# Optimization experiments

Hardware: AMD Instinct MI355X
Metric: run time of the kernel (lower is better)

The kernel has to match this reference:

```python
import jax, jax.numpy as jnp
import numpy as np

B, E, D, P, H = 8192, 100, 300, 100, 20  # batch, experts, embed, projection, hidden

def setup_inputs() -> dict:
    key = jax.random.key(0)
    ks = jax.random.split(key, 10)
    return {
        "x": jax.random.normal(ks[0], (B, D), dtype=jnp.float32),
        "y": jax.random.normal(ks[1], (B, D), dtype=jnp.float32),
        "tag": jax.random.uniform(ks[2], (B, 1), dtype=jnp.float32),
        "weights_1": jax.random.normal(ks[3], (E, D, P), dtype=jnp.float32) * (2.0 / (D + P)) ** 0.5,
        "bias_1": jax.random.normal(ks[4], (E, P), dtype=jnp.float32) * 0.1,
        "hidden_weights": jax.random.normal(ks[5], (E, 2 * P + 2, H), dtype=jnp.float32) * 0.07,
        "hidden_bias": jax.random.normal(ks[6], (E, H), dtype=jnp.float32),
        "outlayer_weights": jax.random.normal(ks[7], (E, H, 1), dtype=jnp.float32) * 0.3,
        "outlayer_bias": jax.random.uniform(ks[8], (E, 1), dtype=jnp.float32),
        "weights_all": jax.random.normal(ks[9], (D, E), dtype=jnp.float32) * (2.0 / (D + E)) ** 0.5,
    }

def reference(x, y, tag, weights_1, bias_1, hidden_weights, hidden_bias,
              outlayer_weights, outlayer_bias, weights_all):
    eps = 1e-8
    # gating: softmax((x+y) @ W_all) over experts  -> [B, E, 1]
    w = jax.nn.softmax((x + y) @ weights_all, axis=1)[:, :, None]
    # per-expert projections: [B, E, P]
    xp = jnp.einsum('bd,edp->bep', x, weights_1) + bias_1
    yp = jnp.einsum('bd,edp->bep', y, weights_1) + bias_1
    # cosine similarity along projection dim (torch semantics: clamp each norm)
    nx = jnp.maximum(jnp.sqrt(jnp.sum(xp * xp, axis=2)), eps)
    ny = jnp.maximum(jnp.sqrt(jnp.sum(yp * yp, axis=2)), eps)
    cos = jnp.sum(xp * yp, axis=2) / (nx * ny)  # [B, E]
    tag_rep = jnp.broadcast_to(tag[:, None, :], (x.shape[0], weights_1.shape[0], tag.shape[1]))
    feat = jnp.concatenate([cos[:, :, None], xp + yp, jnp.abs(xp - yp), tag_rep], axis=2)  # [B,E,2P+2]
    h = jax.nn.relu(jnp.einsum('bef,efh->beh', feat, hidden_weights) + hidden_bias)  # [B,E,H]
    d = jnp.einsum('beh,eho->beo', h, outlayer_weights) + outlayer_bias  # [B,E,1]
    probs = jnp.squeeze(jnp.sum(w * d, axis=1), axis=-1)  # [B]
    return probs
```

## Files before the change

kernel.cpp:

```cpp
#include <hip/hip_runtime.h>
#include <math.h>

#define B_ 8192
#define E_ 100
#define D_ 300
#define P_ 100
#define H_ 20
#define F_ 202
#define NT 10
#define NWG 12800

typedef __attribute__((ext_vector_type(8))) short bf16x8;
typedef __attribute__((ext_vector_type(8))) _Float16 f16x8;
typedef __attribute__((ext_vector_type(4))) float f32x4;
typedef __attribute__((ext_vector_type(8))) unsigned short us8;

#define WG_OFF 0
#define AB_OFF 3276800
#define W1_OFF (AB_OFF + 20971520)
#define WH2_OFF (W1_OFF + 14336000)
#define PD_OFF (WH2_OFF + 1856000)
#define WS_ALL (PD_OFF + 3276800)

__device__ __forceinline__ unsigned short f2bf(float f) {
    unsigned int u = __float_as_uint(f);
    u = (u + 0x7FFF + ((u >> 16) & 1)) >> 16;
    return (unsigned short)u;
}
__device__ __forceinline__ float bf2f(unsigned short h) {
    return __uint_as_float(((unsigned int)h) << 16);
}

#define GLOAD16(g, l) \
    __builtin_amdgcn_global_load_lds((const __attribute__((address_space(1))) unsigned int*)(g), \
                                     (__attribute__((address_space(3))) unsigned int*)(l), 16, 0, 0)

__global__ __launch_bounds__(256) void prep_xy(const float* __restrict__ x,
                                               const float* __restrict__ y,
                                               unsigned short* __restrict__ ab2)
{
    const int bi = blockIdx.x;
    const int rb = bi / NT, t = bi - rb * NT;
    for (int s = threadIdx.x; s < 512; s += 256) {
        const int kg = s >> 7, row = s & 127;
        const float* src = ((row < 64) ? x : y) + (size_t)(rb * 64 + (row & 63)) * D_;
        const int k0 = t * 32 + kg * 8;
        us8 hi, lo;
        #pragma unroll
        for (int j = 0; j < 8; ++j) {
            const int k = k0 + j;
            const float v = (k < D_) ? src[k] : 0.f;
            const unsigned short h = f2bf(v);
            hi[j] = h;
            lo[j] = f2bf(v - bf2f(h));
        }
        unsigned short* tb = ab2 + (size_t)bi * 8192;
        *(us8*)(tb + (size_t)s * 8)         = hi;
        *(us8*)(tb + (size_t)(512 + s) * 8) = lo;
    }
}

__global__ __launch_bounds__(256) void prep_w1(const float* __restrict__ w1,
                                               unsigned short* __restrict__ w1b2)
{
    const int bi = blockIdx.x;
    const int e = bi / NT, t = bi - e * NT;
    for (int s = threadIdx.x; s < 448; s += 256) {
        const int kg = s / 112, p = s - kg * 112;
        const int k0 = t * 32 + kg * 8;
        us8 hi, lo;
        #pragma unroll
        for (int j = 0; j < 8; ++j) {
            const int k = k0 + j;
            const float v = (p < P_ && k < D_) ? w1[((size_t)e * D_ + k) * P_ + p] : 0.f;
            const unsigned short h = f2bf(v);
            hi[j] = h;
            lo[j] = f2bf(v - bf2f(h));
        }
        unsigned short* tb = w1b2 + (size_t)bi * 7168;
        *(us8*)(tb + (size_t)s * 8)         = hi;
        *(us8*)(tb + (size_t)(448 + s) * 8) = lo;
    }
}

__global__ __launch_bounds__(256) void prep_wh(const float* __restrict__ wh,
                                               _Float16* __restrict__ wh2)
{
    const int e = blockIdx.x;
    for (int k = threadIdx.x; k < 20 * 232; k += 256) {
        const int h = k / 232, f = k - h * 232;
        const float v = (f < F_) ? wh[((size_t)e * F_ + f) * H_ + h] : 0.f;
        const _Float16 vh = (_Float16)v;
        wh2[(size_t)e * 9280 + k]        = vh;
        wh2[(size_t)e * 9280 + 4640 + k] = (_Float16)(v - (float)vh);
    }
}

__global__ __launch_bounds__(128) void gate_kernel(
    const float* __restrict__ x, const float* __restrict__ y,
    const float* __restrict__ wall, float* __restrict__ wgate)
{
    __shared__ float s[D_];
    __shared__ float zv[128];
    __shared__ float red[128];
    const int b = blockIdx.x;
    const int tid = threadIdx.x;

    for (int d = tid; d < D_; d += 128)
        s[d] = x[(size_t)b * D_ + d] + y[(size_t)b * D_ + d];
    __syncthreads();

    float acc = 0.f;
    if (tid < E_)
        for (int d = 0; d < D_; ++d) acc += s[d] * wall[(size_t)d * E_ + tid];
    zv[tid] = (tid < E_) ? acc : -INFINITY;
    red[tid] = zv[tid];
    __syncthreads();
    for (int st = 64; st > 0; st >>= 1) {
        if (tid < st) red[tid] = fmaxf(red[tid], red[tid + st]);
        __syncthreads();
    }
    const float m = red[0];
    __syncthreads();
    const float ev = (tid < E_) ? expf(zv[tid] - m) : 0.f;
    red[tid] = ev;
    __syncthreads();
    for (int st = 64; st > 0; st >>= 1) {
        if (tid < st) red[tid] += red[tid + st];
        __syncthreads();
    }
    if (tid < E_) wgate[(size_t)b * E_ + tid] = ev / red[0];
}

template<int MODE>
__global__ __launch_bounds__(256, (MODE == 1) ? 4 : 3) void moe_mfma_kernel(
    const float* __restrict__ tag,
    const unsigned short* __restrict__ ab2,
    const unsigned short* __restrict__ w1b2,
    const _Float16* __restrict__ wh2g,
    const float* __restrict__ b1,
    const float* __restrict__ wh,
    const float* __restrict__ hb,
    const float* __restrict__ wo,
    const float* __restrict__ ob,
    const float* __restrict__ wgate,
    float* __restrict__ pd,
    float* __restrict__ out)
{
    __shared__ __align__(16) char smem[(MODE == 1) ? 29696 : 48256];
    unsigned short (*Bw_lds)[7168] = (unsigned short (*)[7168])smem;
    _Float16 (*featl)[232] = (_Float16 (*)[232])smem;
    _Float16 (*swh2)[20][232] = (_Float16 (*)[20][232])(smem + 29696);

    const int tid  = threadIdx.x;
    const int lane = tid & 63, w = tid >> 6;

    const int bid = blockIdx.x;
    const int rb = ((bid & 7) << 4) | ((bid >> 3) & 15);
    const int e  = bid >> 7;
    const int b0 = rb * 64;
    const int li = lane & 15, kgq = lane >> 4;

    if constexpr (MODE == 0) {
        for (int k = tid; k < 20 * 232; k += 256) {
            const int h = k / 232, f = k - h * 232;
            const float v = (f < F_) ? wh[((size_t)e * F_ + f) * H_ + h] : 0.f;
            const _Float16 vh = (_Float16)v;
            (*swh2)[h][f] = vh;
            swh2[1][h][f] = (_Float16)(v - (float)vh);
        }
    }

    f32x4 accx[7], accy[7];
    #pragma unroll
    for (int ni = 0; ni < 7; ++ni) {
        accx[ni] = (f32x4){0.f, 0.f, 0.f, 0.f};
        accy[ni] = (f32x4){0.f, 0.f, 0.f, 0.f};
    }

    const int a_base = (kgq * 128 + w * 16 + li) * 8;
    const int b_base = (kgq * 112 + li) * 8;

    bf16x8 areg[2][4];
    auto loadA = [&](int kt, int pb) {
        const unsigned short* tb = ab2 + (size_t)(rb * NT + kt) * 8192 + a_base;
        areg[pb][0] = *(const bf16x8*)(tb);
        areg[pb][1] = *(const bf16x8*)(tb + 4096);
        areg[pb][2] = *(const bf16x8*)(tb + 512);
        areg[pb][3] = *(const bf16x8*)(tb + 4608);
    };
    auto stageB = [&](int tt, int bb) {
        const unsigned short* bbase = w1b2 + (size_t)(e * NT + tt) * 7168 + lane * 8;
        #pragma unroll
        for (int k = 0; k < 4; ++k) {
            const int i = w + 4 * k;
            if (i < 14) GLOAD16(bbase + i * 512, &Bw_lds[bb][i * 512]);
        }
    };

    stageB(0, 0);
    loadA(0, 0);
    __syncthreads();
    #pragma unroll
    for (int kt = 0; kt < NT; ++kt) {
        const int cb = kt & 1, nb = cb ^ 1;
        if (kt < NT - 1) {
            stageB(kt + 1, nb);
            loadA(kt + 1, nb);
        }
        const bf16x8 axh = areg[cb][0];
        const bf16x8 axl = areg[cb][1];
        const bf16x8 ayh = areg[cb][2];
        const bf16x8 ayl = areg[cb][3];
        #pragma unroll
        for (int ni = 0; ni < 7; ++ni) {
            const bf16x8 bh = *(const bf16x8*)(&Bw_lds[cb][b_base + ni * 128]);
            const bf16x8 bl = *(const bf16x8*)(&Bw_lds[cb][b_base + ni * 128 + 3584]);
            accx[ni] = __builtin_amdgcn_mfma_f32_16x16x32_bf16(axh, bh, accx[ni], 0, 0, 0);
            accx[ni] = __builtin_amdgcn_mfma_f32_16x16x32_bf16(axl, bh, accx[ni], 0, 0, 0);
            accx[ni] = __builtin_amdgcn_mfma_f32_16x16x32_bf16(axh, bl, accx[ni], 0, 0, 0);
            accy[ni] = __builtin_amdgcn_mfma_f32_16x16x32_bf16(ayh, bh, accy[ni], 0, 0, 0);
            accy[ni] = __builtin_amdgcn_mfma_f32_16x16x32_bf16(ayl, bh, accy[ni], 0, 0, 0);
            accy[ni] = __builtin_amdgcn_mfma_f32_16x16x32_bf16(ayh, bl, accy[ni], 0, 0, 0);
        }
        __syncthreads();
    }

    for (int k = tid; k < 64 * 30; k += 256) featl[k / 30][202 + k % 30] = (_Float16)0.f;

    float pxx[4] = {0, 0, 0, 0}, pyy[4] = {0, 0, 0, 0}, pxy[4] = {0, 0, 0, 0};
    #pragma unroll
    for (int ni = 0; ni < 7; ++ni) {
        const int c = ni * 16 + li;
        if (c < P_) {
            const float bp = b1[(size_t)e * P_ + c];
            #pragma unroll
            for (int j = 0; j < 4; ++j) {
                const float xv = accx[ni][j] + bp;
                const float yv = accy[ni][j] + bp;
                const int r = w * 16 + kgq * 4 + j;
                featl[r][1 + c]   = (_Float16)(xv + yv);
                featl[r][101 + c] = (_Float16)fabsf(xv - yv);
                pxx[j] += xv * xv; pyy[j] += yv * yv; pxy[j] += xv * yv;
            }
        }
    }
    #pragma unroll
    for (int j = 0; j < 4; ++j) {
        #pragma unroll
        for (int m = 1; m < 16; m <<= 1) {
            pxx[j] += __shfl_xor(pxx[j], m);
            pyy[j] += __shfl_xor(pyy[j], m);
            pxy[j] += __shfl_xor(pxy[j], m);
        }
    }
    if (li == 0) {
        #pragma unroll
        for (int j = 0; j < 4; ++j) {
            const int r = w * 16 + kgq * 4 + j;
            const float nx = fmaxf(sqrtf(pxx[j]), 1e-8f);
            const float ny = fmaxf(sqrtf(pyy[j]), 1e-8f);
            featl[r][0]   = (_Float16)(pxy[j] / (nx * ny));
            featl[r][201] = (_Float16)tag[b0 + r];
        }
    }
    __syncthreads();

    const int h1 = 16 + li;
    const bool v1 = (h1 < H_);
    const int h1c = v1 ? h1 : (H_ - 1);
    const _Float16* whp = wh2g + (size_t)e * 9280;

    f32x4 acc0 = (f32x4){0.f, 0.f, 0.f, 0.f};
    f32x4 acc1 = (f32x4){0.f, 0.f, 0.f, 0.f};
    #pragma unroll
    for (int kt = 0; kt < 7; ++kt) {
        const int ko = kt * 32 + kgq * 8;
        const f16x8 af = *(const f16x8*)(&featl[w * 16 + li][ko]);
        f16x8 b0h, b0l, b1h, b1l;
        if constexpr (MODE == 1) {
            b0h = *(const f16x8*)(whp + li * 232 + ko);
            b0l = *(const f16x8*)(whp + 4640 + li * 232 + ko);
            b1h = *(const f16x8*)(whp + h1c * 232 + ko);
            b1l = *(const f16x8*)(whp + 4640 + h1c * 232 + ko);
        } else {
            b0h = *(const f16x8*)(&(*swh2)[li][ko]);
            b0l = *(const f16x8*)(&swh2[1][li][ko]);
            b1h = *(const f16x8*)(&(*swh2)[h1c][ko]);
            b1l = *(const f16x8*)(&swh2[1][h1c][ko]);
        }
        if (!v1) {
            b1h = (f16x8)(_Float16)0.f;
            b1l = (f16x8)(_Float16)0.f;
        }
        acc0 = __builtin_amdgcn_mfma_f32_16x16x32_f16(af, b0h, acc0, 0, 0, 0);
        acc0 = __builtin_amdgcn_mfma_f32_16x16x32_f16(af, b0l, acc0, 0, 0, 0);
        acc1 = __builtin_amdgcn_mfma_f32_16x16x32_f16(af, b1h, acc1, 0, 0, 0);
        acc1 = __builtin_amdgcn_mfma_f32_16x16x32_f16(af, b1l, acc1, 0, 0, 0);
    }

    const float hb0 = hb[(size_t)e * H_ + li];
    const float wo0 = wo[(size_t)e * H_ + li];
    const float hb1 = v1 ? hb[(size_t)e * H_ + h1] : 0.f;
    const float wo1 = v1 ? wo[(size_t)e * H_ + h1] : 0.f;
    #pragma unroll
    for (int j = 0; j < 4; ++j) {
        float t = fmaxf(acc0[j] + hb0, 0.f) * wo0;
        if (v1) t += fmaxf(acc1[j] + hb1, 0.f) * wo1;
        t += __shfl_xor(t, 1);
        t += __shfl_xor(t, 2);
        t += __shfl_xor(t, 4);
        t += __shfl_xor(t, 8);
        if (li == 0) {
            const int r = w * 16 + kgq * 4 + j;
            const int b = b0 + r;
            const float v = wgate[(size_t)b * E_ + e] * (t + ob[e]);
            if (MODE == 1) pd[(size_t)e * B_ + b] = v;
            else           atomicAdd(&out[b], v);
        }
    }
}

__global__ __launch_bounds__(256) void reduce_kernel(const float* __restrict__ pd,
                                                     float* __restrict__ out)
{
    const int b = blockIdx.x * 256 + threadIdx.x;
    float s = 0.f;
    for (int e = 0; e < E_; ++e) s += pd[(size_t)e * B_ + b];
    out[b] = s;
}

extern "C" void kernel_launch(void* const* d_in, const int* in_sizes, int n_in,
                              void* d_out, int out_size, void* d_ws, size_t ws_size,
                              hipStream_t stream)
{
    const float* x    = (const float*)d_in[0];
    const float* y    = (const float*)d_in[1];
    const float* tag  = (const float*)d_in[2];
    const float* w1   = (const float*)d_in[3];
    const float* b1   = (const float*)d_in[4];
    const float* wh   = (const float*)d_in[5];
    const float* hb   = (const float*)d_in[6];
    const float* wo   = (const float*)d_in[7];
    const float* ob   = (const float*)d_in[8];
    const float* wall = (const float*)d_in[9];

    float* out = (float*)d_out;
    char* ws = (char*)d_ws;
    float*          wgate = (float*)(ws + WG_OFF);
    unsigned short* ab2   = (unsigned short*)(ws + AB_OFF);
    unsigned short* w1b2  = (unsigned short*)(ws + W1_OFF);
    _Float16*       wh2   = (_Float16*)(ws + WH2_OFF);
    float*          pd    = (float*)(ws + PD_OFF);

    const bool full = (ws_size >= (size_t)WS_ALL);

    prep_xy<<<dim3(128 * NT), dim3(256), 0, stream>>>(x, y, ab2);
    prep_w1<<<dim3(E_ * NT), dim3(256), 0, stream>>>(w1, w1b2);
    gate_kernel<<<dim3(B_), dim3(128), 0, stream>>>(x, y, wall, wgate);

    if (full) {
        prep_wh<<<dim3(E_), dim3(256), 0, stream>>>(wh, wh2);
        moe_mfma_kernel<1><<<dim3(NWG), dim3(256), 0, stream>>>(
            tag, ab2, w1b2, wh2, b1, wh, hb, wo, ob, wgate, pd, out);
        reduce_kernel<<<dim3(B_ / 256), dim3(256), 0, stream>>>(pd, out);
    } else {
        hipMemsetAsync(out, 0, (size_t)B_ * sizeof(float), stream);
        moe_mfma_kernel<0><<<dim3(NWG), dim3(256), 0, stream>>>(
            tag, ab2, w1b2, wh2, b1, wh, hb, wo, ob, wgate, pd, out);
    }
}
```

Measured before the change: 406.7 us.

## Drop LDS staging of W1 tiles and load MFMA operands directly from global

Removes the double-buffered global_load_lds staging of the W1 tile and the A-operand register prefetch, so the first-stage GEMM reads both operands straight from global memory with no per-iteration block barriers. LDS shrinks to the feature buffer alone, and the barrier after the feature writes goes away because each wave now reads only the rows it wrote itself. The MODE 0 path now builds the hidden-weight hi/lo f16 split from strided global loads inside the MFMA loop instead of a shared-memory preload. The aim is less LDS use and fewer barriers, at the cost of losing latency hiding and reuse of the W1 tile across the four waves, which now each fetch it from cache.

```diff
diff --git a/kernel.cpp b/kernel.cpp
--- a/kernel.cpp
+++ b/kernel.cpp
@@ -30,10 +30,6 @@
 __device__ __forceinline__ float bf2f(unsigned short h) {
     return __uint_as_float(((unsigned int)h) << 16);
 }
-
-#define GLOAD16(g, l) \
-    __builtin_amdgcn_global_load_lds((const __attribute__((address_space(1))) unsigned int*)(g), \
-                                     (__attribute__((address_space(3))) unsigned int*)(l), 16, 0, 0)
 
 __global__ __launch_bounds__(256) void prep_xy(const float* __restrict__ x,
                                                const float* __restrict__ y,
@@ -133,7 +129,7 @@
 }
 
 template<int MODE>
-__global__ __launch_bounds__(256, (MODE == 1) ? 4 : 3) void moe_mfma_kernel(
+__global__ __launch_bounds__(256, 3) void moe_mfma_kernel(
     const float* __restrict__ tag,
     const unsigned short* __restrict__ ab2,
     const unsigned short* __restrict__ w1b2,
@@ -147,10 +143,7 @@
     float* __restrict__ pd,
     float* __restrict__ out)
 {
-    __shared__ __align__(16) char smem[(MODE == 1) ? 29696 : 48256];
-    unsigned short (*Bw_lds)[7168] = (unsigned short (*)[7168])smem;
-    _Float16 (*featl)[232] = (_Float16 (*)[232])smem;
-    _Float16 (*swh2)[20][232] = (_Float16 (*)[20][232])(smem + 29696);
+    __shared__ __align__(16) _Float16 featl[64][232];
 
     const int tid  = threadIdx.x;
     const int lane = tid & 63, w = tid >> 6;
@@ -161,16 +154,6 @@
     const int b0 = rb * 64;
     const int li = lane & 15, kgq = lane >> 4;
 
-    if constexpr (MODE == 0) {
-        for (int k = tid; k < 20 * 232; k += 256) {
-            const int h = k / 232, f = k - h * 232;
-            const float v = (f < F_) ? wh[((size_t)e * F_ + f) * H_ + h] : 0.f;
-            const _Float16 vh = (_Float16)v;
-            (*swh2)[h][f] = vh;
-            swh2[1][h][f] = (_Float16)(v - (float)vh);
-        }
-    }
-
     f32x4 accx[7], accy[7];
     #pragma unroll
     for (int ni = 0; ni < 7; ++ni) {
@@ -180,42 +163,21 @@
 
     const int a_base = (kgq * 128 + w * 16 + li) * 8;
     const int b_base = (kgq * 112 + li) * 8;
-
-    bf16x8 areg[2][4];
-    auto loadA = [&](int kt, int pb) {
-        const unsigned short* tb = ab2 + (size_t)(rb * NT + kt) * 8192 + a_base;
-        areg[pb][0] = *(const bf16x8*)(tb);
-        areg[pb][1] = *(const bf16x8*)(tb + 4096);
-        areg[pb][2] = *(const bf16x8*)(tb + 512);
-        areg[pb][3] = *(const bf16x8*)(tb + 4608);
-    };
-    auto stageB = [&](int tt, int bb) {
-        const unsigned short* bbase = w1b2 + (size_t)(e * NT + tt) * 7168 + lane * 8;
-        #pragma unroll
-        for (int k = 0; k < 4; ++k) {
-            const int i = w + 4 * k;
-            if (i < 14) GLOAD16(bbase + i * 512, &Bw_lds[bb][i * 512]);
-        }
-    };
-
-    stageB(0, 0);
-    loadA(0, 0);
-    __syncthreads();
+    const unsigned short* aptr = ab2 + (size_t)rb * NT * 8192 + a_base;
+    const unsigned short* bptr = w1b2 + (size_t)e * NT * 7168 + b_base;
+
     #pragma unroll
     for (int kt = 0; kt < NT; ++kt) {
-        const int cb = kt & 1, nb = cb ^ 1;
-        if (kt < NT - 1) {
-            stageB(kt + 1, nb);
-            loadA(kt + 1, nb);
-        }
-        const bf16x8 axh = areg[cb][0];
-        const bf16x8 axl = areg[cb][1];
-        const bf16x8 ayh = areg[cb][2];
-        const bf16x8 ayl = areg[cb][3];
+        const unsigned short* ak = aptr + kt * 8192;
+        const unsigned short* bk = bptr + kt * 7168;
+        const bf16x8 axh = *(const bf16x8*)(ak);
+        const bf16x8 axl = *(const bf16x8*)(ak + 4096);
+        const bf16x8 ayh = *(const bf16x8*)(ak + 512);
+        const bf16x8 ayl = *(const bf16x8*)(ak + 4608);
         #pragma unroll
         for (int ni = 0; ni < 7; ++ni) {
-            const bf16x8 bh = *(const bf16x8*)(&Bw_lds[cb][b_base + ni * 128]);
-            const bf16x8 bl = *(const bf16x8*)(&Bw_lds[cb][b_base + ni * 128 + 3584]);
+            const bf16x8 bh = *(const bf16x8*)(bk + ni * 128);
+            const bf16x8 bl = *(const bf16x8*)(bk + ni * 128 + 3584);
             accx[ni] = __builtin_amdgcn_mfma_f32_16x16x32_bf16(axh, bh, accx[ni], 0, 0, 0);
             accx[ni] = __builtin_amdgcn_mfma_f32_16x16x32_bf16(axl, bh, accx[ni], 0, 0, 0);
             accx[ni] = __builtin_amdgcn_mfma_f32_16x16x32_bf16(axh, bl, accx[ni], 0, 0, 0);
@@ -223,10 +185,10 @@
             accy[ni] = __builtin_amdgcn_mfma_f32_16x16x32_bf16(ayl, bh, accy[ni], 0, 0, 0);
             accy[ni] = __builtin_amdgcn_mfma_f32_16x16x32_bf16(ayh, bl, accy[ni], 0, 0, 0);
         }
-        __syncthreads();
-    }
-
-    for (int k = tid; k < 64 * 30; k += 256) featl[k / 30][202 + k % 30] = (_Float16)0.f;
+    }
+
+    for (int idx = lane; idx < 16 * 30; idx += 64)
+        featl[w * 16 + idx / 30][202 + idx % 30] = (_Float16)0.f;
 
     float pxx[4] = {0, 0, 0, 0}, pyy[4] = {0, 0, 0, 0}, pxy[4] = {0, 0, 0, 0};
     #pragma unroll
@@ -264,7 +226,6 @@
             featl[r][201] = (_Float16)tag[b0 + r];
         }
     }
-    __syncthreads();
 
     const int h1 = 16 + li;
     const bool v1 = (h1 < H_);
@@ -284,10 +245,15 @@
             b1h = *(const f16x8*)(whp + h1c * 232 + ko);
             b1l = *(const f16x8*)(whp + 4640 + h1c * 232 + ko);
         } else {
-            b0h = *(const f16x8*)(&(*swh2)[li][ko]);
-            b0l = *(const f16x8*)(&swh2[1][li][ko]);
-            b1h = *(const f16x8*)(&(*swh2)[h1c][ko]);
-            b1l = *(const f16x8*)(&swh2[1][h1c][ko]);
+            #pragma unroll
+            for (int j = 0; j < 8; ++j) {
+                const int f = ko + j;
+                const float v0 = (f < F_) ? wh[((size_t)e * F_ + f) * H_ + li]  : 0.f;
+                const float v1f = (f < F_) ? wh[((size_t)e * F_ + f) * H_ + h1c] : 0.f;
+                const _Float16 v0h = (_Float16)v0, v1h = (_Float16)v1f;
+                b0h[j] = v0h; b0l[j] = (_Float16)(v0 - (float)v0h);
+                b1h[j] = v1h; b1l[j] = (_Float16)(v1f - (float)v1h);
+            }
         }
         if (!v1) {
             b1h = (f16x8)(_Float16)0.f;
```

New measurement: 676.7 us. +66.4%, slower.

## Process two row blocks per workgroup to reuse staged expert weights

Applied to the files above, without the earlier changes.

Each workgroup now computes two 64-row batch blocks for one expert, which halves the grid. The B-weight tile staged into LDS is reused across both row blocks, and the accumulators are doubled. The MODE 0 path no longer stages hidden weights into LDS; it reads and splits them from global memory into registers for each k-step. The cost is higher register and LDS use, with occupancy bounded at 2, and fewer workgroups to hide latency.

```diff
diff --git a/kernel.cpp b/kernel.cpp
--- a/kernel.cpp
+++ b/kernel.cpp
@@ -8,7 +8,7 @@
 #define H_ 20
 #define F_ 202
 #define NT 10
-#define NWG 12800
+#define NWG 6400
 
 typedef __attribute__((ext_vector_type(8))) short bf16x8;
 typedef __attribute__((ext_vector_type(8))) _Float16 f16x8;
@@ -133,7 +133,7 @@
 }
 
 template<int MODE>
-__global__ __launch_bounds__(256, (MODE == 1) ? 4 : 3) void moe_mfma_kernel(
+__global__ __launch_bounds__(256, 2) void moe_mfma_kernel(
     const float* __restrict__ tag,
     const unsigned short* __restrict__ ab2,
     const unsigned short* __restrict__ w1b2,
@@ -147,47 +147,42 @@
     float* __restrict__ pd,
     float* __restrict__ out)
 {
-    __shared__ __align__(16) char smem[(MODE == 1) ? 29696 : 48256];
+    __shared__ __align__(16) char smem[59392];
     unsigned short (*Bw_lds)[7168] = (unsigned short (*)[7168])smem;
     _Float16 (*featl)[232] = (_Float16 (*)[232])smem;
-    _Float16 (*swh2)[20][232] = (_Float16 (*)[20][232])(smem + 29696);
 
     const int tid  = threadIdx.x;
     const int lane = tid & 63, w = tid >> 6;
 
     const int bid = blockIdx.x;
-    const int rb = ((bid & 7) << 4) | ((bid >> 3) & 15);
-    const int e  = bid >> 7;
-    const int b0 = rb * 64;
+    const int xcd = bid & 7;
+    const int rbp = (bid >> 3) & 7;
+    const int e   = bid >> 6;
+    const int rb0 = (xcd << 4) | (rbp << 1);
     const int li = lane & 15, kgq = lane >> 4;
 
-    if constexpr (MODE == 0) {
-        for (int k = tid; k < 20 * 232; k += 256) {
-            const int h = k / 232, f = k - h * 232;
-            const float v = (f < F_) ? wh[((size_t)e * F_ + f) * H_ + h] : 0.f;
-            const _Float16 vh = (_Float16)v;
-            (*swh2)[h][f] = vh;
-            swh2[1][h][f] = (_Float16)(v - (float)vh);
-        }
-    }
-
-    f32x4 accx[7], accy[7];
-    #pragma unroll
-    for (int ni = 0; ni < 7; ++ni) {
-        accx[ni] = (f32x4){0.f, 0.f, 0.f, 0.f};
-        accy[ni] = (f32x4){0.f, 0.f, 0.f, 0.f};
-    }
+    f32x4 accx[2][7], accy[2][7];
+    #pragma unroll
+    for (int rbi = 0; rbi < 2; ++rbi)
+        #pragma unroll
+        for (int ni = 0; ni < 7; ++ni) {
+            accx[rbi][ni] = (f32x4){0.f, 0.f, 0.f, 0.f};
+            accy[rbi][ni] = (f32x4){0.f, 0.f, 0.f, 0.f};
+        }
 
     const int a_base = (kgq * 128 + w * 16 + li) * 8;
     const int b_base = (kgq * 112 + li) * 8;
 
-    bf16x8 areg[2][4];
+    bf16x8 areg[2][2][4];
     auto loadA = [&](int kt, int pb) {
-        const unsigned short* tb = ab2 + (size_t)(rb * NT + kt) * 8192 + a_base;
-        areg[pb][0] = *(const bf16x8*)(tb);
-        areg[pb][1] = *(const bf16x8*)(tb + 4096);
-        areg[pb][2] = *(const bf16x8*)(tb + 512);
-        areg[pb][3] = *(const bf16x8*)(tb + 4608);
+        #pragma unroll
+        for (int rbi = 0; rbi < 2; ++rbi) {
+            const unsigned short* tb = ab2 + (size_t)((rb0 + rbi) * NT + kt) * 8192 + a_base;
+            areg[pb][rbi][0] = *(const bf16x8*)(tb);
+            areg[pb][rbi][1] = *(const bf16x8*)(tb + 4096);
+            areg[pb][rbi][2] = *(const bf16x8*)(tb + 512);
+            areg[pb][rbi][3] = *(const bf16x8*)(tb + 4608);
+        }
     };
     auto stageB = [&](int tt, int bb) {
         const unsigned short* bbase = w1b2 + (size_t)(e * NT + tt) * 7168 + lane * 8;
@@ -208,61 +203,67 @@
             stageB(kt + 1, nb);
             loadA(kt + 1, nb);
         }
-        const bf16x8 axh = areg[cb][0];
-        const bf16x8 axl = areg[cb][1];
-        const bf16x8 ayh = areg[cb][2];
-        const bf16x8 ayl = areg[cb][3];
         #pragma unroll
         for (int ni = 0; ni < 7; ++ni) {
             const bf16x8 bh = *(const bf16x8*)(&Bw_lds[cb][b_base + ni * 128]);
             const bf16x8 bl = *(const bf16x8*)(&Bw_lds[cb][b_base + ni * 128 + 3584]);
-            accx[ni] = __builtin_amdgcn_mfma_f32_16x16x32_bf16(axh, bh, accx[ni], 0, 0, 0);
-            accx[ni] = __builtin_amdgcn_mfma_f32_16x16x32_bf16(axl, bh, accx[ni], 0, 0, 0);
-            accx[ni] = __builtin_amdgcn_mfma_f32_16x16x32_bf16(axh, bl, accx[ni], 0, 0, 0);
-            accy[ni] = __builtin_amdgcn_mfma_f32_16x16x32_bf16(ayh, bh, accy[ni], 0, 0, 0);
-            accy[ni] = __builtin_amdgcn_mfma_f32_16x16x32_bf16(ayl, bh, accy[ni], 0, 0, 0);
-            accy[ni] = __builtin_amdgcn_mfma_f32_16x16x32_bf16(ayh, bl, accy[ni], 0, 0, 0);
+            #pragma unroll
+            for (int rbi = 0; rbi < 2; ++rbi) {
+                accx[rbi][ni] = __builtin_amdgcn_mfma_f32_16x16x32_bf16(areg[cb][rbi][0], bh, accx[rbi][ni], 0, 0, 0);
+                accx[rbi][ni] = __builtin_amdgcn_mfma_f32_16x16x32_bf16(areg[cb][rbi][1], bh, accx[rbi][ni], 0, 0, 0);
+                accx[rbi][ni] = __builtin_amdgcn_mfma_f32_16x16x32_bf16(areg[cb][rbi][0], bl, accx[rbi][ni], 0, 0, 0);
+                accy[rbi][ni] = __builtin_amdgcn_mfma_f32_16x16x32_bf16(areg[cb][rbi][2], bh, accy[rbi][ni], 0, 0, 0);
+                accy[rbi][ni] = __builtin_amdgcn_mfma_f32_16x16x32_bf16(areg[cb][rbi][3], bh, accy[rbi][ni], 0, 0, 0);
+                accy[rbi][ni] = __builtin_amdgcn_mfma_f32_16x16x32_bf16(areg[cb][rbi][2], bl, accy[rbi][ni], 0, 0, 0);
+            }
         }
         __syncthreads();
     }
 
-    for (int k = tid; k < 64 * 30; k += 256) featl[k / 30][202 + k % 30] = (_Float16)0.f;
-
-    float pxx[4] = {0, 0, 0, 0}, pyy[4] = {0, 0, 0, 0}, pxy[4] = {0, 0, 0, 0};
+    for (int k = tid; k < 128 * 30; k += 256) featl[k / 30][202 + k % 30] = (_Float16)0.f;
+
+    float pxx[2][4] = {{0}}, pyy[2][4] = {{0}}, pxy[2][4] = {{0}};
     #pragma unroll
     for (int ni = 0; ni < 7; ++ni) {
         const int c = ni * 16 + li;
         if (c < P_) {
             const float bp = b1[(size_t)e * P_ + c];
             #pragma unroll
+            for (int rbi = 0; rbi < 2; ++rbi) {
+                #pragma unroll
+                for (int j = 0; j < 4; ++j) {
+                    const float xv = accx[rbi][ni][j] + bp;
+                    const float yv = accy[rbi][ni][j] + bp;
+                    const int r = w * 16 + kgq * 4 + j;
+                    featl[rbi * 64 + r][1 + c]   = (_Float16)(xv + yv);
+                    featl[rbi * 64 + r][101 + c] = (_Float16)fabsf(xv - yv);
+                    pxx[rbi][j] += xv * xv; pyy[rbi][j] += yv * yv; pxy[rbi][j] += xv * yv;
+                }
+            }
+        }
+    }
+    #pragma unroll
+    for (int rbi = 0; rbi < 2; ++rbi)
+        #pragma unroll
+        for (int j = 0; j < 4; ++j) {
+            #pragma unroll
+            for (int m = 1; m < 16; m <<= 1) {
+                pxx[rbi][j] += __shfl_xor(pxx[rbi][j], m);
+                pyy[rbi][j] += __shfl_xor(pyy[rbi][j], m);
+                pxy[rbi][j] += __shfl_xor(pxy[rbi][j], m);
+            }
+        }
+    if (li == 0) {
+        #pragma unroll
+        for (int rbi = 0; rbi < 2; ++rbi)
+            #pragma unroll
             for (int j = 0; j < 4; ++j) {
-                const float xv = accx[ni][j] + bp;
-                const float yv = accy[ni][j] + bp;
                 const int r = w * 16 + kgq * 4 + j;
-                featl[r][1 + c]   = (_Float16)(xv + yv);
-                featl[r][101 + c] = (_Float16)fabsf(xv - yv);
-                pxx[j] += xv * xv; pyy[j] += yv * yv; pxy[j] += xv * yv;
-            }
-        }
-    }
-    #pragma unroll
-    for (int j = 0; j < 4; ++j) {
-        #pragma unroll
-        for (int m = 1; m < 16; m <<= 1) {
-            pxx[j] += __shfl_xor(pxx[j], m);
-            pyy[j] += __shfl_xor(pyy[j], m);
-            pxy[j] += __shfl_xor(pxy[j], m);
-        }
-    }
-    if (li == 0) {
-        #pragma unroll
-        for (int j = 0; j < 4; ++j) {
-            const int r = w * 16 + kgq * 4 + j;
-            const float nx = fmaxf(sqrtf(pxx[j]), 1e-8f);
-            const float ny = fmaxf(sqrtf(pyy[j]), 1e-8f);
-            featl[r][0]   = (_Float16)(pxy[j] / (nx * ny));
-            featl[r][201] = (_Float16)tag[b0 + r];
-        }
+                const float nx = fmaxf(sqrtf(pxx[rbi][j]), 1e-8f);
+                const float ny = fmaxf(sqrtf(pyy[rbi][j]), 1e-8f);
+                featl[rbi * 64 + r][0]   = (_Float16)(pxy[rbi][j] / (nx * ny));
+                featl[rbi * 64 + r][201] = (_Float16)tag[(rb0 + rbi) * 64 + r];
+            }
     }
     __syncthreads();
 
@@ -271,12 +272,15 @@
     const int h1c = v1 ? h1 : (H_ - 1);
     const _Float16* whp = wh2g + (size_t)e * 9280;
 
-    f32x4 acc0 = (f32x4){0.f, 0.f, 0.f, 0.f};
-    f32x4 acc1 = (f32x4){0.f, 0.f, 0.f, 0.f};
+    f32x4 accC[2][2];
+    #pragma unroll
+    for (int rbi = 0; rbi < 2; ++rbi) {
+        accC[rbi][0] = (f32x4){0.f, 0.f, 0.f, 0.f};
+        accC[rbi][1] = (f32x4){0.f, 0.f, 0.f, 0.f};
+    }
     #pragma unroll
     for (int kt = 0; kt < 7; ++kt) {
         const int ko = kt * 32 + kgq * 8;
-        const f16x8 af = *(const f16x8*)(&featl[w * 16 + li][ko]);
         f16x8 b0h, b0l, b1h, b1l;
         if constexpr (MODE == 1) {
             b0h = *(const f16x8*)(whp + li * 232 + ko);
@@ -284,19 +288,28 @@
             b1h = *(const f16x8*)(whp + h1c * 232 + ko);
             b1l = *(const f16x8*)(whp + 4640 + h1c * 232 + ko);
         } else {
-            b0h = *(const f16x8*)(&(*swh2)[li][ko]);
-            b0l = *(const f16x8*)(&swh2[1][li][ko]);
-            b1h = *(const f16x8*)(&(*swh2)[h1c][ko]);
-            b1l = *(const f16x8*)(&swh2[1][h1c][ko]);
+            #pragma unroll
+            for (int j = 0; j < 8; ++j) {
+                const int f = ko + j;
+                const float v0  = (f < F_) ? wh[((size_t)e * F_ + f) * H_ + li]  : 0.f;
+                const float v1f = (f < F_) ? wh[((size_t)e * F_ + f) * H_ + h1c] : 0.f;
+                const _Float16 v0h = (_Float16)v0, v1h = (_Float16)v1f;
+                b0h[j] = v0h; b0l[j] = (_Float16)(v0 - (float)v0h);
+                b1h[j] = v1h; b1l[j] = (_Float16)(v1f - (float)v1h);
+            }
         }
         if (!v1) {
             b1h = (f16x8)(_Float16)0.f;
             b1l = (f16x8)(_Float16)0.f;
         }
-        acc0 = __builtin_amdgcn_mfma_f32_16x16x32_f16(af, b0h, acc0, 0, 0, 0);
-        acc0 = __builtin_amdgcn_mfma_f32_16x16x32_f16(af, b0l, acc0, 0, 0, 0);
-        acc1 = __builtin_amdgcn_mfma_f32_16x16x32_f16(af, b1h, acc1, 0, 0, 0);
-        acc1 = __builtin_amdgcn_mfma_f32_16x16x32_f16(af, b1l, acc1, 0, 0, 0);
+        #pragma unroll
+        for (int rbi = 0; rbi < 2; ++rbi) {
+            const f16x8 af = *(const f16x8*)(&featl[rbi * 64 + w * 16 + li][ko]);
+            accC[rbi][0] = __builtin_amdgcn_mfma_f32_16x16x32_f16(af, b0h, accC[rbi][0], 0, 0, 0);
+            accC[rbi][0] = __builtin_amdgcn_mfma_f32_16x16x32_f16(af, b0l, accC[rbi][0], 0, 0, 0);
+            accC[rbi][1] = __builtin_amdgcn_mfma_f32_16x16x32_f16(af, b1h, accC[rbi][1], 0, 0, 0);
+            accC[rbi][1] = __builtin_amdgcn_mfma_f32_16x16x32_f16(af, b1l, accC[rbi][1], 0, 0, 0);
+        }
     }
 
     const float hb0 = hb[(size_t)e * H_ + li];
@@ -304,21 +317,23 @@
     const float hb1 = v1 ? hb[(size_t)e * H_ + h1] : 0.f;
     const float wo1 = v1 ? wo[(size_t)e * H_ + h1] : 0.f;
     #pragma unroll
-    for (int j = 0; j < 4; ++j) {
-        float t = fmaxf(acc0[j] + hb0, 0.f) * wo0;
-        if (v1) t += fmaxf(acc1[j] + hb1, 0.f) * wo1;
-        t += __shfl_xor(t, 1);
-        t += __shfl_xor(t, 2);
-        t += __shfl_xor(t, 4);
-        t += __shfl_xor(t, 8);
-        if (li == 0) {
-            const int r = w * 16 + kgq * 4 + j;
-            const int b = b0 + r;
-            const float v = wgate[(size_t)b * E_ + e] * (t + ob[e]);
-            if (MODE == 1) pd[(size_t)e * B_ + b] = v;
-            else           atomicAdd(&out[b], v);
-        }
-    }
+    for (int rbi = 0; rbi < 2; ++rbi)
+        #pragma unroll
+        for (int j = 0; j < 4; ++j) {
+            float t = fmaxf(accC[rbi][0][j] + hb0, 0.f) * wo0;
+            if (v1) t += fmaxf(accC[rbi][1][j] + hb1, 0.f) * wo1;
+            t += __shfl_xor(t, 1);
+            t += __shfl_xor(t, 2);
+            t += __shfl_xor(t, 4);
+            t += __shfl_xor(t, 8);
+            if (li == 0) {
+                const int r = w * 16 + kgq * 4 + j;
+                const int b = (rb0 + rbi) * 64 + r;
+                const float v = wgate[(size_t)b * E_ + e] * (t + ob[e]);
+                if (MODE == 1) pd[(size_t)e * B_ + b] = v;
+                else           atomicAdd(&out[b], v);
+            }
+        }
 }
 
 __global__ __launch_bounds__(256) void reduce_kernel(const float* __restrict__ pd,
```

After: 408.6 us. About the same (+0.5%).

## Tile gate kernel over 32 rows with shared W_all and drop a block barrier

Applied to the files above, without the earlier changes.

The gating kernel now handles 32 batch rows per block instead of one. It stages x+y and chunks of W_all in shared memory and has each thread compute 13 expert logits, with the softmax reduced by warp shuffles rather than shared-memory tree reductions. This is meant to cut repeated global reads of W_all and the per-row barrier overhead. In the MoE kernel, each wave now zeroes only its own feature-row padding, which lets the block-wide barrier before the hidden-layer MFMA be removed. That removal relies on each wave reading only featl rows it wrote itself, and the code shows this holds because the later MFMA A-operand rows are w*16+li.

```diff
diff --git a/kernel.cpp b/kernel.cpp
--- a/kernel.cpp
+++ b/kernel.cpp
@@ -96,40 +96,67 @@
     }
 }
 
-__global__ __launch_bounds__(128) void gate_kernel(
+__global__ __launch_bounds__(256) void gate_kernel(
     const float* __restrict__ x, const float* __restrict__ y,
     const float* __restrict__ wall, float* __restrict__ wgate)
 {
-    __shared__ float s[D_];
-    __shared__ float zv[128];
-    __shared__ float red[128];
-    const int b = blockIdx.x;
+    __shared__ float swall[75][104];
+    __shared__ float ss[32][76];
     const int tid = threadIdx.x;
-
-    for (int d = tid; d < D_; d += 128)
-        s[d] = x[(size_t)b * D_ + d] + y[(size_t)b * D_ + d];
-    __syncthreads();
-
-    float acc = 0.f;
-    if (tid < E_)
-        for (int d = 0; d < D_; ++d) acc += s[d] * wall[(size_t)d * E_ + tid];
-    zv[tid] = (tid < E_) ? acc : -INFINITY;
-    red[tid] = zv[tid];
-    __syncthreads();
-    for (int st = 64; st > 0; st >>= 1) {
-        if (tid < st) red[tid] = fmaxf(red[tid], red[tid + st]);
+    const int r = tid >> 3, g = tid & 7;
+    const int b0 = blockIdx.x * 32;
+
+    float z[13];
+    #pragma unroll
+    for (int i = 0; i < 13; ++i) z[i] = 0.f;
+
+    for (int dc = 0; dc < D_; dc += 75) {
         __syncthreads();
-    }
-    const float m = red[0];
-    __syncthreads();
-    const float ev = (tid < E_) ? expf(zv[tid] - m) : 0.f;
-    red[tid] = ev;
-    __syncthreads();
-    for (int st = 64; st > 0; st >>= 1) {
-        if (tid < st) red[tid] += red[tid + st];
+        for (int k = tid; k < 32 * 75; k += 256) {
+            const int rr = k / 75, dd = k - rr * 75;
+            ss[rr][dd] = x[(size_t)(b0 + rr) * D_ + dc + dd]
+                       + y[(size_t)(b0 + rr) * D_ + dc + dd];
+        }
+        for (int k = tid; k < 75 * 104; k += 256) {
+            const int dd = k / 104, e = k - dd * 104;
+            swall[dd][e] = (e < E_) ? wall[(size_t)(dc + dd) * E_ + e] : 0.f;
+        }
         __syncthreads();
-    }
-    if (tid < E_) wgate[(size_t)b * E_ + tid] = ev / red[0];
+        for (int dd = 0; dd < 75; ++dd) {
+            const float sv = ss[r][dd];
+            #pragma unroll
+            for (int i = 0; i < 13; ++i)
+                z[i] += sv * swall[dd][g * 13 + i];
+        }
+    }
+    #pragma unroll
+    for (int i = 0; i < 13; ++i)
+        if (g * 13 + i >= E_) z[i] = -INFINITY;
+
+    float m = z[0];
+    #pragma unroll
+    for (int i = 1; i < 13; ++i) m = fmaxf(m, z[i]);
+    m = fmaxf(m, __shfl_xor(m, 1));
+    m = fmaxf(m, __shfl_xor(m, 2));
+    m = fmaxf(m, __shfl_xor(m, 4));
+
+    float ev[13];
+    float sum = 0.f;
+    #pragma unroll
+    for (int i = 0; i < 13; ++i) {
+        ev[i] = (g * 13 + i < E_) ? expf(z[i] - m) : 0.f;
+        sum += ev[i];
+    }
+    sum += __shfl_xor(sum, 1);
+    sum += __shfl_xor(sum, 2);
+    sum += __shfl_xor(sum, 4);
+
+    const int b = b0 + r;
+    #pragma unroll
+    for (int i = 0; i < 13; ++i) {
+        const int e = g * 13 + i;
+        if (e < E_) wgate[(size_t)b * E_ + e] = ev[i] / sum;
+    }
 }
 
 template<int MODE>
@@ -226,7 +253,8 @@
         __syncthreads();
     }
 
-    for (int k = tid; k < 64 * 30; k += 256) featl[k / 30][202 + k % 30] = (_Float16)0.f;
+    for (int idx = lane; idx < 16 * 30; idx += 64)
+        featl[w * 16 + idx / 30][202 + idx % 30] = (_Float16)0.f;
 
     float pxx[4] = {0, 0, 0, 0}, pyy[4] = {0, 0, 0, 0}, pxy[4] = {0, 0, 0, 0};
     #pragma unroll
@@ -264,7 +292,6 @@
             featl[r][201] = (_Float16)tag[b0 + r];
         }
     }
-    __syncthreads();
 
     const int h1 = 16 + li;
     const bool v1 = (h1 < H_);
@@ -357,7 +384,7 @@
 
     prep_xy<<<dim3(128 * NT), dim3(256), 0, stream>>>(x, y, ab2);
     prep_w1<<<dim3(E_ * NT), dim3(256), 0, stream>>>(w1, w1b2);
-    gate_kernel<<<dim3(B_), dim3(128), 0, stream>>>(x, y, wall, wgate);
+    gate_kernel<<<dim3(B_ / 32), dim3(256), 0, stream>>>(x, y, wall, wgate);
 
     if (full) {
         prep_wh<<<dim3(E_), dim3(256), 0, stream>>>(wh, wh2);
```

Measured after the change: 432.9 us. 6.4% more time.
